# Optimization experiments

Hardware: AMD Instinct MI355X
Metric: run time of the kernel (lower is better)

## Reference

```python
import jax, jax.numpy as jnp
import numpy as np

DT = 0.01
G = 9.81
M = 1.5
E3 = jnp.array([0.0, 0.0, 1.0], dtype=jnp.float32)
K = 8388608


def setup_inputs() -> dict:
    key = jax.random.key(0)
    k1, k2, k3 = jax.random.split(key, 3)
    f = jax.random.normal(k1, (K, 3), dtype=jnp.float32)
    p_0 = jax.random.normal(k2, (3,), dtype=jnp.float32)
    v_0 = jax.random.normal(k3, (3,), dtype=jnp.float32)
    return {"f": f, "p_0": p_0, "v_0": v_0}


def reference(f, p_0, v_0):
    K_ = f.shape[0]
    # Original loop: v[0] uses f[0]; v[i+1] uses f[i]  =>  f index per step: [0, 0, 1, ..., K-2]
    idx = jnp.concatenate([jnp.zeros(1, dtype=jnp.int32), jnp.arange(K_ - 1, dtype=jnp.int32)])
    a = (DT / M) * f[idx] - (DT * G) * E3          # [K,3] per-step velocity increment
    v = v_0[None, :] + jnp.cumsum(a, axis=0)       # [K,3]
    v_prev = jnp.concatenate([v_0[None, :], v[:-1]], axis=0)
    p = p_0[None, :] + (DT / 2) * jnp.cumsum(v + v_prev, axis=0)  # trapezoidal position
    return (p, v)
```

## Files before the change

### kernel.cpp

```cpp
#include <hip/hip_runtime.h>


namespace {
constexpr int  KE    = 8388608;
constexpr int  CHUNK = 2048;
constexpr int  NB    = KE / CHUNK;
constexpr int  BLOCK = 256;
constexpr int  R     = CHUNK / BLOCK;
constexpr int  NF4   = 3 * CHUNK / 4;
constexpr int  PRET  = 1024;
constexpr int  BPT   = NB / PRET;
constexpr float DTc = 0.01f;
constexpr float Cc  = 0.01f / 1.5f;
constexpr float GZ  = -0.01f * 9.81f;
typedef float f32x4 __attribute__((ext_vector_type(4)));
__device__ __forceinline__ int physf4(int q) { return 7 * (q / 6) + q % 6; }
}

__global__ __launch_bounds__(BLOCK) void k_agg(const float* __restrict__ f,
                                               float* __restrict__ W) {
  const int b = blockIdx.x, t = threadIdx.x;
  const int lane = t & 63, wid = t >> 6;
  const float4* src = (const float4*)(f + (size_t)3 * CHUNK * b);
  float A[3] = {0.f, 0.f, 0.f}, Bw[3] = {0.f, 0.f, 0.f};
#pragma unroll
  for (int it = 0; it < 2; ++it) {
    int q3 = it * BLOCK + t;
    float4 d0 = src[3 * q3], d1 = src[3 * q3 + 1], d2 = src[3 * q3 + 2];
    float j0 = (float)(4 * q3), j1 = j0 + 1.f, j2 = j0 + 2.f, j3 = j0 + 3.f;
    A[0] += d0.x; Bw[0] += j0 * d0.x;  A[1] += d0.y; Bw[1] += j0 * d0.y;  A[2] += d0.z; Bw[2] += j0 * d0.z;
    A[0] += d0.w; Bw[0] += j1 * d0.w;  A[1] += d1.x; Bw[1] += j1 * d1.x;  A[2] += d1.y; Bw[2] += j1 * d1.y;
    A[0] += d1.z; Bw[0] += j2 * d1.z;  A[1] += d1.w; Bw[1] += j2 * d1.w;  A[2] += d2.x; Bw[2] += j2 * d2.x;
    A[0] += d2.y; Bw[0] += j3 * d2.y;  A[1] += d2.z; Bw[1] += j3 * d2.z;  A[2] += d2.w; Bw[2] += j3 * d2.w;
  }
#pragma unroll
  for (int d = 32; d >= 1; d >>= 1) {
#pragma unroll
    for (int q = 0; q < 3; ++q) {
      A[q]  += __shfl_down(A[q], d);
      Bw[q] += __shfl_down(Bw[q], d);
    }
  }
  __shared__ float wag[4][6];
  if (lane == 0) {
#pragma unroll
    for (int q = 0; q < 3; ++q) { wag[wid][q] = A[q]; wag[wid][3 + q] = Bw[q]; }
  }
  __syncthreads();
  if (t == 0) {
#pragma unroll
    for (int q = 0; q < 3; ++q) {
      W[q * NB + b]       = wag[0][q] + wag[1][q] + wag[2][q] + wag[3][q];
      W[(3 + q) * NB + b] = wag[0][3 + q] + wag[1][3 + q] + wag[2][3 + q] + wag[3][3 + q];
    }
  }
}

__global__ __launch_bounds__(PRET) void k_pre(const float* __restrict__ W,
                                              float* __restrict__ W2) {
  const int t = threadIdx.x, lane = t & 63, wid = t >> 6;
  double Ac[BPT][3], Wc[BPT][3];
#pragma unroll
  for (int k = 0; k < BPT; ++k) {
    const int c = BPT * t + k;
#pragma unroll
    for (int q = 0; q < 3; ++q) {
      double a  = (double)W[q * NB + c];
      double bw = (double)W[(3 + q) * NB + c];
      Ac[k][q] = a;
      Wc[k][q] = (double)(CHUNK - 1) * a - bw;
    }
  }
  double tA[3] = {0, 0, 0}, tW[3] = {0, 0, 0};
#pragma unroll
  for (int k = 0; k < BPT; ++k) {
#pragma unroll
    for (int q = 0; q < 3; ++q) {
      tW[q] += (double)((BPT - 1 - k) * CHUNK) * Ac[k][q] + Wc[k][q];
      tA[q] += Ac[k][q];
    }
  }
#pragma unroll
  for (int d = 1; d < 64; d <<= 1) {
    double pA[3], pW[3];
#pragma unroll
    for (int q = 0; q < 3; ++q) { pA[q] = __shfl_up(tA[q], d); pW[q] = __shfl_up(tW[q], d); }
    if (lane >= d) {
      const double Ld = (double)(d * BPT * CHUNK);
#pragma unroll
      for (int q = 0; q < 3; ++q) { tW[q] = pW[q] + Ld * pA[q] + tW[q]; tA[q] += pA[q]; }
    }
  }
  double eA[3], eW[3];
#pragma unroll
  for (int q = 0; q < 3; ++q) { eA[q] = __shfl_up(tA[q], 1); eW[q] = __shfl_up(tW[q], 1); }
  if (lane == 0) {
#pragma unroll
    for (int q = 0; q < 3; ++q) { eA[q] = 0.0; eW[q] = 0.0; }
  }
  __shared__ double wagd[16][6];
  if (lane == 63) {
#pragma unroll
    for (int q = 0; q < 3; ++q) { wagd[wid][q] = tA[q]; wagd[wid][3 + q] = tW[q]; }
  }
  __syncthreads();
  double oA[3] = {0, 0, 0}, oW[3] = {0, 0, 0};
  for (int w = 0; w < wid; ++w) {
#pragma unroll
    for (int q = 0; q < 3; ++q) oW[q] = oW[q] + (double)(64 * BPT * CHUNK) * oA[q] + wagd[w][3 + q];
#pragma unroll
    for (int q = 0; q < 3; ++q) oA[q] += wagd[w][q];
  }
  double Ex[3], Hx[3];
#pragma unroll
  for (int q = 0; q < 3; ++q) {
    Ex[q] = oA[q] + eA[q];
    Hx[q] = oW[q] + (double)(lane * BPT * CHUNK) * oA[q] + eW[q];
  }
#pragma unroll
  for (int k = 0; k < BPT; ++k) {
    const int c = BPT * t + k;
#pragma unroll
    for (int q = 0; q < 3; ++q) {
      W2[6 * c + q]     = (float)Ex[q];
      W2[6 * c + 3 + q] = (float)Hx[q];
      Hx[q] += (double)CHUNK * Ex[q] + Wc[k][q];
      Ex[q] += Ac[k][q];
    }
  }
}

__global__ __launch_bounds__(BLOCK, 5) void k_scan(const float* __restrict__ f,
                                                   const float* __restrict__ W2,
                                                   const float* __restrict__ p0v,
                                                   const float* __restrict__ v0v,
                                                   float* __restrict__ out) {
  const int b = blockIdx.x, t = threadIdx.x;
  const int lane = t & 63, wid = t >> 6;
  const long start = (long)b * CHUNK;

  __shared__ f32x4 buf[7 * BLOCK];
  __shared__ float wag[4][6];

  {
    const f32x4* src = (const f32x4*)(f + 3 * start);
#pragma unroll
    for (int it = 0; it < 6; ++it) {
      const int q = t + BLOCK * it;
      buf[physf4(q)] = src[q];
    }
  }
  __syncthreads();

  float z[3 * R];
#pragma unroll
  for (int u = 0; u < 6; ++u) {
    f32x4 d = buf[7 * t + u];
    z[4 * u] = d.x; z[4 * u + 1] = d.y; z[4 * u + 2] = d.z; z[4 * u + 3] = d.w;
  }

  float tS[3] = {0, 0, 0}, tT[3] = {0, 0, 0};
#pragma unroll
  for (int e = 0; e < R; ++e) {
    const float wt = (float)(R - 1 - e);
#pragma unroll
    for (int q = 0; q < 3; ++q) { float v = z[3 * e + q]; tS[q] += v; tT[q] += wt * v; }
  }
#pragma unroll
  for (int d = 1; d < 64; d <<= 1) {
    float pS[3], pT[3];
#pragma unroll
    for (int q = 0; q < 3; ++q) { pS[q] = __shfl_up(tS[q], d); pT[q] = __shfl_up(tT[q], d); }
    if (lane >= d) {
      const float Ld = (float)(R * d);
#pragma unroll
      for (int q = 0; q < 3; ++q) { tT[q] = pT[q] + Ld * pS[q] + tT[q]; tS[q] += pS[q]; }
    }
  }
  float eS[3], eT[3];
#pragma unroll
  for (int q = 0; q < 3; ++q) { eS[q] = __shfl_up(tS[q], 1); eT[q] = __shfl_up(tT[q], 1); }
  if (lane == 0) {
#pragma unroll
    for (int q = 0; q < 3; ++q) { eS[q] = 0.f; eT[q] = 0.f; }
  }
  if (lane == 63) {
#pragma unroll
    for (int q = 0; q < 3; ++q) { wag[wid][q] = tS[q]; wag[wid][3 + q] = tT[q]; }
  }
  __syncthreads();
  float oS[3] = {0, 0, 0}, oT[3] = {0, 0, 0};
  for (int w = 0; w < wid; ++w) {
#pragma unroll
    for (int q = 0; q < 3; ++q) oT[q] = oT[q] + 512.0f * oS[q] + wag[w][3 + q];
#pragma unroll
    for (int q = 0; q < 3; ++q) oS[q] += wag[w][q];
  }
  float E0[3], H0[3];
#pragma unroll
  for (int q = 0; q < 3; ++q) {
    const float Eg = W2[6 * b + q], Hg = W2[6 * b + 3 + q];
    E0[q] = Eg + oS[q] + eS[q];
    H0[q] = Hg + (float)(R * t) * Eg + (oT[q] + (float)(R * lane) * oS[q] + eT[q]);
  }

  const float f0[3] = {f[0], f[1], f[2]};
  const float p0x = p0v[0], p0y = p0v[1], p0z = p0v[2];
  const float v0x = v0v[0], v0y = v0v[1], v0z = v0v[2];
  const float a1 = DTc * Cc, a2 = 0.5f * DTc * Cc, c3 = 0.5f * DTc * GZ;

  float lsum[3] = {0, 0, 0};
  float runH[3] = {H0[0], H0[1], H0[2]};
  float ve[3 * R];
#pragma unroll
  for (int g = 0; g < 2; ++g) {
    float pe[12];
#pragma unroll
    for (int e4 = 0; e4 < 4; ++e4) {
      const int e = 4 * g + e4;
      const float n1 = (float)(int)(start + t * R + e + 1);
      float S_[3], T_[3];
#pragma unroll
      for (int q = 0; q < 3; ++q) {
        const float curE = E0[q] + lsum[q];
        runH[q] += curE;
        S_[q] = f0[q] + curE;
        T_[q] = n1 * f0[q] + runH[q];
        lsum[q] += z[3 * e + q];
      }
      ve[3 * e + 0] = v0x + Cc * S_[0];
      ve[3 * e + 1] = v0y + Cc * S_[1];
      ve[3 * e + 2] = v0z + Cc * S_[2] + GZ * n1;
      pe[3 * e4 + 0] = p0x + DTc * n1 * v0x + a1 * T_[0] - a2 * S_[0];
      pe[3 * e4 + 1] = p0y + DTc * n1 * v0y + a1 * T_[1] - a2 * S_[1];
      pe[3 * e4 + 2] = p0z + DTc * n1 * v0z + a1 * T_[2] - a2 * S_[2] + c3 * n1 * n1;
    }
#pragma unroll
    for (int u = 0; u < 3; ++u) {
      f32x4 pv = {pe[4 * u], pe[4 * u + 1], pe[4 * u + 2], pe[4 * u + 3]};
      buf[7 * t + 3 * g + u] = pv;
    }
  }
  __syncthreads();

  {
    f32x4* dst = (f32x4*)out + (size_t)NF4 * b;
#pragma unroll
    for (int it = 0; it < 6; ++it) {
      const int q = t + BLOCK * it;
      f32x4 d = buf[physf4(q)];
      __builtin_nontemporal_store(d, dst + q);
    }
  }
  __syncthreads();

#pragma unroll
  for (int u = 0; u < 6; ++u) {
    f32x4 vv = {ve[4 * u], ve[4 * u + 1], ve[4 * u + 2], ve[4 * u + 3]};
    buf[7 * t + u] = vv;
  }
  __syncthreads();
  {
    f32x4* dst = (f32x4*)(out + (size_t)3 * KE) + (size_t)NF4 * b;
#pragma unroll
    for (int it = 0; it < 6; ++it) {
      const int q = t + BLOCK * it;
      f32x4 d = buf[physf4(q)];
      __builtin_nontemporal_store(d, dst + q);
    }
  }
}

extern "C" void kernel_launch(void* const* d_in, const int* in_sizes, int n_in,
                              void* d_out, int out_size, void* d_ws, size_t ws_size,
                              hipStream_t stream) {
  const float* f  = (const float*)d_in[0];
  const float* p0 = (const float*)d_in[1];
  const float* v0 = (const float*)d_in[2];
  float* out = (float*)d_out;
  float* W   = (float*)d_ws;
  float* W2  = W + 6 * NB;
  k_agg <<<NB, BLOCK, 0, stream>>>(f, W);
  k_pre <<<1, PRET, 0, stream>>>(W, W2);
  k_scan<<<NB, BLOCK, 0, stream>>>(f, W2, p0, v0, out);
}
```

Before: 75.65 us.

## Halve chunk size, load inputs directly to registers, stage p and v together

Chunk size drops from 2048 to 1024 elements, so each thread handles 4 elements instead of 8 and the grid doubles. The scan kernel now reads f straight from global memory into registers instead of staging it through shared memory, and writes both position and velocity tiles to shared memory in one pass, removing two barriers. k_pre no longer keeps per-chunk values in registers; it re-reads W from global memory in the output loop, cutting register pressure at the cost of extra loads. The direct per-thread loads of 48 contiguous bytes are less coalesced than the old strided pattern, and the larger grid adds launch and block overhead.

```diff
diff --git a/kernel.cpp b/kernel.cpp
--- a/kernel.cpp
+++ b/kernel.cpp
@@ -3,7 +3,7 @@
 
 namespace {
 constexpr int  KE    = 8388608;
-constexpr int  CHUNK = 2048;
+constexpr int  CHUNK = 1024;
 constexpr int  NB    = KE / CHUNK;
 constexpr int  BLOCK = 256;
 constexpr int  R     = CHUNK / BLOCK;
@@ -14,24 +14,20 @@
 constexpr float Cc  = 0.01f / 1.5f;
 constexpr float GZ  = -0.01f * 9.81f;
 typedef float f32x4 __attribute__((ext_vector_type(4)));
-__device__ __forceinline__ int physf4(int q) { return 7 * (q / 6) + q % 6; }
 }
 
 __global__ __launch_bounds__(BLOCK) void k_agg(const float* __restrict__ f,
                                                float* __restrict__ W) {
   const int b = blockIdx.x, t = threadIdx.x;
   const int lane = t & 63, wid = t >> 6;
-  const float4* src = (const float4*)(f + (size_t)3 * CHUNK * b);
-  float A[3] = {0.f, 0.f, 0.f}, Bw[3] = {0.f, 0.f, 0.f};
-#pragma unroll
-  for (int it = 0; it < 2; ++it) {
-    int q3 = it * BLOCK + t;
-    float4 d0 = src[3 * q3], d1 = src[3 * q3 + 1], d2 = src[3 * q3 + 2];
-    float j0 = (float)(4 * q3), j1 = j0 + 1.f, j2 = j0 + 2.f, j3 = j0 + 3.f;
-    A[0] += d0.x; Bw[0] += j0 * d0.x;  A[1] += d0.y; Bw[1] += j0 * d0.y;  A[2] += d0.z; Bw[2] += j0 * d0.z;
-    A[0] += d0.w; Bw[0] += j1 * d0.w;  A[1] += d1.x; Bw[1] += j1 * d1.x;  A[2] += d1.y; Bw[2] += j1 * d1.y;
-    A[0] += d1.z; Bw[0] += j2 * d1.z;  A[1] += d1.w; Bw[1] += j2 * d1.w;  A[2] += d2.x; Bw[2] += j2 * d2.x;
-    A[0] += d2.y; Bw[0] += j3 * d2.y;  A[1] += d2.z; Bw[1] += j3 * d2.z;  A[2] += d2.w; Bw[2] += j3 * d2.w;
+  const f32x4* src = (const f32x4*)(f + (size_t)3 * CHUNK * b);
+  float A[3], Bw[3];
+  {
+    f32x4 d0 = src[3 * t], d1 = src[3 * t + 1], d2 = src[3 * t + 2];
+    const float j0 = (float)(4 * t), j1 = j0 + 1.f, j2 = j0 + 2.f, j3 = j0 + 3.f;
+    A[0] = d0.x + d0.w + d1.z + d2.y;  Bw[0] = j0 * d0.x + j1 * d0.w + j2 * d1.z + j3 * d2.y;
+    A[1] = d0.y + d1.x + d1.w + d2.z;  Bw[1] = j0 * d0.y + j1 * d1.x + j2 * d1.w + j3 * d2.z;
+    A[2] = d0.z + d1.y + d2.x + d2.w;  Bw[2] = j0 * d0.z + j1 * d1.y + j2 * d2.x + j3 * d2.w;
   }
 #pragma unroll
   for (int d = 32; d >= 1; d >>= 1) {
@@ -59,25 +55,17 @@
 __global__ __launch_bounds__(PRET) void k_pre(const float* __restrict__ W,
                                               float* __restrict__ W2) {
   const int t = threadIdx.x, lane = t & 63, wid = t >> 6;
-  double Ac[BPT][3], Wc[BPT][3];
+  double tA[3] = {0, 0, 0}, tW[3] = {0, 0, 0};
 #pragma unroll
   for (int k = 0; k < BPT; ++k) {
     const int c = BPT * t + k;
 #pragma unroll
     for (int q = 0; q < 3; ++q) {
-      double a  = (double)W[q * NB + c];
-      double bw = (double)W[(3 + q) * NB + c];
-      Ac[k][q] = a;
-      Wc[k][q] = (double)(CHUNK - 1) * a - bw;
-    }
-  }
-  double tA[3] = {0, 0, 0}, tW[3] = {0, 0, 0};
-#pragma unroll
-  for (int k = 0; k < BPT; ++k) {
-#pragma unroll
-    for (int q = 0; q < 3; ++q) {
-      tW[q] += (double)((BPT - 1 - k) * CHUNK) * Ac[k][q] + Wc[k][q];
-      tA[q] += Ac[k][q];
+      const double a  = (double)W[q * NB + c];
+      const double bw = (double)W[(3 + q) * NB + c];
+      const double wc = (double)(CHUNK - 1) * a - bw;
+      tW[q] += (double)((BPT - 1 - k) * CHUNK) * a + wc;
+      tA[q] += a;
     }
   }
 #pragma unroll
@@ -124,8 +112,11 @@
     for (int q = 0; q < 3; ++q) {
       W2[6 * c + q]     = (float)Ex[q];
       W2[6 * c + 3 + q] = (float)Hx[q];
-      Hx[q] += (double)CHUNK * Ex[q] + Wc[k][q];
-      Ex[q] += Ac[k][q];
+      const double a  = (double)W[q * NB + c];
+      const double bw = (double)W[(3 + q) * NB + c];
+      const double wc = (double)(CHUNK - 1) * a - bw;
+      Hx[q] += (double)CHUNK * Ex[q] + wc;
+      Ex[q] += a;
     }
   }
 }
@@ -142,21 +133,14 @@
   __shared__ f32x4 buf[7 * BLOCK];
   __shared__ float wag[4][6];
 
-  {
-    const f32x4* src = (const f32x4*)(f + 3 * start);
-#pragma unroll
-    for (int it = 0; it < 6; ++it) {
-      const int q = t + BLOCK * it;
-      buf[physf4(q)] = src[q];
-    }
-  }
-  __syncthreads();
-
   float z[3 * R];
-#pragma unroll
-  for (int u = 0; u < 6; ++u) {
-    f32x4 d = buf[7 * t + u];
-    z[4 * u] = d.x; z[4 * u + 1] = d.y; z[4 * u + 2] = d.z; z[4 * u + 3] = d.w;
+  {
+    const f32x4* src = (const f32x4*)(f + 3 * start) + 3 * t;
+#pragma unroll
+    for (int u = 0; u < 3; ++u) {
+      f32x4 d = src[u];
+      z[4 * u] = d.x; z[4 * u + 1] = d.y; z[4 * u + 2] = d.z; z[4 * u + 3] = d.w;
+    }
   }
 
   float tS[3] = {0, 0, 0}, tT[3] = {0, 0, 0};
@@ -192,7 +176,7 @@
   float oS[3] = {0, 0, 0}, oT[3] = {0, 0, 0};
   for (int w = 0; w < wid; ++w) {
 #pragma unroll
-    for (int q = 0; q < 3; ++q) oT[q] = oT[q] + 512.0f * oS[q] + wag[w][3 + q];
+    for (int q = 0; q < 3; ++q) oT[q] = oT[q] + 256.0f * oS[q] + wag[w][3 + q];
 #pragma unroll
     for (int q = 0; q < 3; ++q) oS[q] += wag[w][q];
   }
@@ -211,61 +195,50 @@
 
   float lsum[3] = {0, 0, 0};
   float runH[3] = {H0[0], H0[1], H0[2]};
-  float ve[3 * R];
-#pragma unroll
-  for (int g = 0; g < 2; ++g) {
-    float pe[12];
-#pragma unroll
-    for (int e4 = 0; e4 < 4; ++e4) {
-      const int e = 4 * g + e4;
-      const float n1 = (float)(int)(start + t * R + e + 1);
-      float S_[3], T_[3];
-#pragma unroll
-      for (int q = 0; q < 3; ++q) {
-        const float curE = E0[q] + lsum[q];
-        runH[q] += curE;
-        S_[q] = f0[q] + curE;
-        T_[q] = n1 * f0[q] + runH[q];
-        lsum[q] += z[3 * e + q];
-      }
-      ve[3 * e + 0] = v0x + Cc * S_[0];
-      ve[3 * e + 1] = v0y + Cc * S_[1];
-      ve[3 * e + 2] = v0z + Cc * S_[2] + GZ * n1;
-      pe[3 * e4 + 0] = p0x + DTc * n1 * v0x + a1 * T_[0] - a2 * S_[0];
-      pe[3 * e4 + 1] = p0y + DTc * n1 * v0y + a1 * T_[1] - a2 * S_[1];
-      pe[3 * e4 + 2] = p0z + DTc * n1 * v0z + a1 * T_[2] - a2 * S_[2] + c3 * n1 * n1;
-    }
-#pragma unroll
-    for (int u = 0; u < 3; ++u) {
-      f32x4 pv = {pe[4 * u], pe[4 * u + 1], pe[4 * u + 2], pe[4 * u + 3]};
-      buf[7 * t + 3 * g + u] = pv;
-    }
+  float pe[12], ve[12];
+#pragma unroll
+  for (int e = 0; e < R; ++e) {
+    const float n1 = (float)(int)(start + t * R + e + 1);
+    float S_[3], T_[3];
+#pragma unroll
+    for (int q = 0; q < 3; ++q) {
+      const float curE = E0[q] + lsum[q];
+      runH[q] += curE;
+      S_[q] = f0[q] + curE;
+      T_[q] = n1 * f0[q] + runH[q];
+      lsum[q] += z[3 * e + q];
+    }
+    ve[3 * e + 0] = v0x + Cc * S_[0];
+    ve[3 * e + 1] = v0y + Cc * S_[1];
+    ve[3 * e + 2] = v0z + Cc * S_[2] + GZ * n1;
+    pe[3 * e + 0] = p0x + DTc * n1 * v0x + a1 * T_[0] - a2 * S_[0];
+    pe[3 * e + 1] = p0y + DTc * n1 * v0y + a1 * T_[1] - a2 * S_[1];
+    pe[3 * e + 2] = p0z + DTc * n1 * v0z + a1 * T_[2] - a2 * S_[2] + c3 * n1 * n1;
+  }
+#pragma unroll
+  for (int u = 0; u < 3; ++u) {
+    f32x4 pv = {pe[4 * u], pe[4 * u + 1], pe[4 * u + 2], pe[4 * u + 3]};
+    f32x4 vv = {ve[4 * u], ve[4 * u + 1], ve[4 * u + 2], ve[4 * u + 3]};
+    buf[7 * t + u]     = pv;
+    buf[7 * t + 3 + u] = vv;
   }
   __syncthreads();
 
   {
     f32x4* dst = (f32x4*)out + (size_t)NF4 * b;
 #pragma unroll
-    for (int it = 0; it < 6; ++it) {
+    for (int it = 0; it < 3; ++it) {
       const int q = t + BLOCK * it;
-      f32x4 d = buf[physf4(q)];
+      f32x4 d = buf[7 * (q / 3) + q % 3];
       __builtin_nontemporal_store(d, dst + q);
     }
   }
-  __syncthreads();
-
-#pragma unroll
-  for (int u = 0; u < 6; ++u) {
-    f32x4 vv = {ve[4 * u], ve[4 * u + 1], ve[4 * u + 2], ve[4 * u + 3]};
-    buf[7 * t + u] = vv;
-  }
-  __syncthreads();
   {
     f32x4* dst = (f32x4*)(out + (size_t)3 * KE) + (size_t)NF4 * b;
 #pragma unroll
-    for (int it = 0; it < 6; ++it) {
+    for (int it = 0; it < 3; ++it) {
       const int q = t + BLOCK * it;
-      f32x4 d = buf[physf4(q)];
+      f32x4 d = buf[7 * (q / 3) + 3 + q % 3];
       __builtin_nontemporal_store(d, dst + q);
     }
   }
```

New measurement: 83.74 us. 10.7% more time.

## Use 512-thread scan blocks with planar LDS staging for p and v

Applied to the files above, without the earlier changes.

The scan kernel now runs 512 threads per block, so each thread handles 4 elements instead of 8. The LDS staging buffer changes from a padded 7-stride layout to three planes per output, which lets p and v be staged together and drops two block barriers plus the second LDS write pass. The larger block raises the wave count and lowers per-thread register pressure. In exchange it uses more LDS per block and adds more cross-wave prefix steps.

```diff
diff --git a/kernel.cpp b/kernel.cpp
--- a/kernel.cpp
+++ b/kernel.cpp
@@ -5,28 +5,29 @@
 constexpr int  KE    = 8388608;
 constexpr int  CHUNK = 2048;
 constexpr int  NB    = KE / CHUNK;
-constexpr int  BLOCK = 256;
-constexpr int  R     = CHUNK / BLOCK;
+constexpr int  ABLK  = 256;
+constexpr int  SBLK  = 512;
+constexpr int  R     = CHUNK / SBLK;
 constexpr int  NF4   = 3 * CHUNK / 4;
+constexpr int  PLANE = NF4 / 3 + 1;
 constexpr int  PRET  = 1024;
 constexpr int  BPT   = NB / PRET;
 constexpr float DTc = 0.01f;
 constexpr float Cc  = 0.01f / 1.5f;
 constexpr float GZ  = -0.01f * 9.81f;
 typedef float f32x4 __attribute__((ext_vector_type(4)));
-__device__ __forceinline__ int physf4(int q) { return 7 * (q / 6) + q % 6; }
-}
-
-__global__ __launch_bounds__(BLOCK) void k_agg(const float* __restrict__ f,
-                                               float* __restrict__ W) {
+}
+
+__global__ __launch_bounds__(ABLK) void k_agg(const float* __restrict__ f,
+                                              float* __restrict__ W) {
   const int b = blockIdx.x, t = threadIdx.x;
   const int lane = t & 63, wid = t >> 6;
-  const float4* src = (const float4*)(f + (size_t)3 * CHUNK * b);
+  const f32x4* src = (const f32x4*)(f + (size_t)3 * CHUNK * b);
   float A[3] = {0.f, 0.f, 0.f}, Bw[3] = {0.f, 0.f, 0.f};
 #pragma unroll
   for (int it = 0; it < 2; ++it) {
-    int q3 = it * BLOCK + t;
-    float4 d0 = src[3 * q3], d1 = src[3 * q3 + 1], d2 = src[3 * q3 + 2];
+    int q3 = it * ABLK + t;
+    f32x4 d0 = src[3 * q3], d1 = src[3 * q3 + 1], d2 = src[3 * q3 + 2];
     float j0 = (float)(4 * q3), j1 = j0 + 1.f, j2 = j0 + 2.f, j3 = j0 + 3.f;
     A[0] += d0.x; Bw[0] += j0 * d0.x;  A[1] += d0.y; Bw[1] += j0 * d0.y;  A[2] += d0.z; Bw[2] += j0 * d0.z;
     A[0] += d0.w; Bw[0] += j1 * d0.w;  A[1] += d1.x; Bw[1] += j1 * d1.x;  A[2] += d1.y; Bw[2] += j1 * d1.y;
@@ -130,32 +131,32 @@
   }
 }
 
-__global__ __launch_bounds__(BLOCK, 5) void k_scan(const float* __restrict__ f,
-                                                   const float* __restrict__ W2,
-                                                   const float* __restrict__ p0v,
-                                                   const float* __restrict__ v0v,
-                                                   float* __restrict__ out) {
+__global__ __launch_bounds__(SBLK, 3) void k_scan(const float* __restrict__ f,
+                                                  const float* __restrict__ W2,
+                                                  const float* __restrict__ p0v,
+                                                  const float* __restrict__ v0v,
+                                                  float* __restrict__ out) {
   const int b = blockIdx.x, t = threadIdx.x;
   const int lane = t & 63, wid = t >> 6;
   const long start = (long)b * CHUNK;
 
-  __shared__ f32x4 buf[7 * BLOCK];
-  __shared__ float wag[4][6];
+  __shared__ f32x4 buf[6 * PLANE];
+  __shared__ float wag[8][6];
 
   {
     const f32x4* src = (const f32x4*)(f + 3 * start);
 #pragma unroll
-    for (int it = 0; it < 6; ++it) {
-      const int q = t + BLOCK * it;
-      buf[physf4(q)] = src[q];
+    for (int it = 0; it < 3; ++it) {
+      const int q = t + SBLK * it;
+      buf[PLANE * (q % 3) + q / 3] = src[q];
     }
   }
   __syncthreads();
 
   float z[3 * R];
 #pragma unroll
-  for (int u = 0; u < 6; ++u) {
-    f32x4 d = buf[7 * t + u];
+  for (int u = 0; u < 3; ++u) {
+    f32x4 d = buf[PLANE * u + t];
     z[4 * u] = d.x; z[4 * u + 1] = d.y; z[4 * u + 2] = d.z; z[4 * u + 3] = d.w;
   }
 
@@ -192,7 +193,7 @@
   float oS[3] = {0, 0, 0}, oT[3] = {0, 0, 0};
   for (int w = 0; w < wid; ++w) {
 #pragma unroll
-    for (int q = 0; q < 3; ++q) oT[q] = oT[q] + 512.0f * oS[q] + wag[w][3 + q];
+    for (int q = 0; q < 3; ++q) oT[q] = oT[q] + 256.0f * oS[q] + wag[w][3 + q];
 #pragma unroll
     for (int q = 0; q < 3; ++q) oS[q] += wag[w][q];
   }
@@ -211,61 +212,50 @@
 
   float lsum[3] = {0, 0, 0};
   float runH[3] = {H0[0], H0[1], H0[2]};
-  float ve[3 * R];
-#pragma unroll
-  for (int g = 0; g < 2; ++g) {
-    float pe[12];
-#pragma unroll
-    for (int e4 = 0; e4 < 4; ++e4) {
-      const int e = 4 * g + e4;
-      const float n1 = (float)(int)(start + t * R + e + 1);
-      float S_[3], T_[3];
-#pragma unroll
-      for (int q = 0; q < 3; ++q) {
-        const float curE = E0[q] + lsum[q];
-        runH[q] += curE;
-        S_[q] = f0[q] + curE;
-        T_[q] = n1 * f0[q] + runH[q];
-        lsum[q] += z[3 * e + q];
-      }
-      ve[3 * e + 0] = v0x + Cc * S_[0];
-      ve[3 * e + 1] = v0y + Cc * S_[1];
-      ve[3 * e + 2] = v0z + Cc * S_[2] + GZ * n1;
-      pe[3 * e4 + 0] = p0x + DTc * n1 * v0x + a1 * T_[0] - a2 * S_[0];
-      pe[3 * e4 + 1] = p0y + DTc * n1 * v0y + a1 * T_[1] - a2 * S_[1];
-      pe[3 * e4 + 2] = p0z + DTc * n1 * v0z + a1 * T_[2] - a2 * S_[2] + c3 * n1 * n1;
-    }
-#pragma unroll
-    for (int u = 0; u < 3; ++u) {
-      f32x4 pv = {pe[4 * u], pe[4 * u + 1], pe[4 * u + 2], pe[4 * u + 3]};
-      buf[7 * t + 3 * g + u] = pv;
-    }
+  float pe[12], ve[12];
+#pragma unroll
+  for (int e = 0; e < R; ++e) {
+    const float n1 = (float)(int)(start + t * R + e + 1);
+    float S_[3], T_[3];
+#pragma unroll
+    for (int q = 0; q < 3; ++q) {
+      const float curE = E0[q] + lsum[q];
+      runH[q] += curE;
+      S_[q] = f0[q] + curE;
+      T_[q] = n1 * f0[q] + runH[q];
+      lsum[q] += z[3 * e + q];
+    }
+    ve[3 * e + 0] = v0x + Cc * S_[0];
+    ve[3 * e + 1] = v0y + Cc * S_[1];
+    ve[3 * e + 2] = v0z + Cc * S_[2] + GZ * n1;
+    pe[3 * e + 0] = p0x + DTc * n1 * v0x + a1 * T_[0] - a2 * S_[0];
+    pe[3 * e + 1] = p0y + DTc * n1 * v0y + a1 * T_[1] - a2 * S_[1];
+    pe[3 * e + 2] = p0z + DTc * n1 * v0z + a1 * T_[2] - a2 * S_[2] + c3 * n1 * n1;
+  }
+#pragma unroll
+  for (int u = 0; u < 3; ++u) {
+    f32x4 pv = {pe[4 * u], pe[4 * u + 1], pe[4 * u + 2], pe[4 * u + 3]};
+    f32x4 vv = {ve[4 * u], ve[4 * u + 1], ve[4 * u + 2], ve[4 * u + 3]};
+    buf[PLANE * u + t]       = pv;
+    buf[PLANE * (3 + u) + t] = vv;
   }
   __syncthreads();
 
   {
     f32x4* dst = (f32x4*)out + (size_t)NF4 * b;
 #pragma unroll
-    for (int it = 0; it < 6; ++it) {
-      const int q = t + BLOCK * it;
-      f32x4 d = buf[physf4(q)];
+    for (int it = 0; it < 3; ++it) {
+      const int q = t + SBLK * it;
+      f32x4 d = buf[PLANE * (q % 3) + q / 3];
       __builtin_nontemporal_store(d, dst + q);
     }
   }
-  __syncthreads();
-
-#pragma unroll
-  for (int u = 0; u < 6; ++u) {
-    f32x4 vv = {ve[4 * u], ve[4 * u + 1], ve[4 * u + 2], ve[4 * u + 3]};
-    buf[7 * t + u] = vv;
-  }
-  __syncthreads();
   {
     f32x4* dst = (f32x4*)(out + (size_t)3 * KE) + (size_t)NF4 * b;
 #pragma unroll
-    for (int it = 0; it < 6; ++it) {
-      const int q = t + BLOCK * it;
-      f32x4 d = buf[physf4(q)];
+    for (int it = 0; it < 3; ++it) {
+      const int q = t + SBLK * it;
+      f32x4 d = buf[PLANE * (3 + q % 3) + q / 3];
       __builtin_nontemporal_store(d, dst + q);
     }
   }
@@ -280,7 +270,7 @@
   float* out = (float*)d_out;
   float* W   = (float*)d_ws;
   float* W2  = W + 6 * NB;
-  k_agg <<<NB, BLOCK, 0, stream>>>(f, W);
+  k_agg <<<NB, ABLK, 0, stream>>>(f, W);
   k_pre <<<1, PRET, 0, stream>>>(W, W2);
-  k_scan<<<NB, BLOCK, 0, stream>>>(f, W2, p0, v0, out);
-}
+  k_scan<<<NB, SBLK, 0, stream>>>(f, W2, p0, v0, out);
+}
```

Result: slower. 78.00 us (+3.1%).

## Fuse chunk aggregation and prefix pass via last-block atomic counter

Applied to the files above, without the earlier changes.

Merges the per-chunk aggregation kernel and the single-block prefix kernel into one launch. Each block publishes its partial sums and increments a global counter, and the last block to arrive does the cross-chunk prefix scan with 256 threads instead of 1024. This removes one kernel launch and its gap, but adds a memset launch, and the serial tail now runs on fewer threads with more work per thread. It also hoists the W2 and scalar loads to the top of the scan kernel so their latency overlaps the shared-memory staging.

```diff
diff --git a/kernel.cpp b/kernel.cpp
--- a/kernel.cpp
+++ b/kernel.cpp
@@ -8,8 +8,7 @@
 constexpr int  BLOCK = 256;
 constexpr int  R     = CHUNK / BLOCK;
 constexpr int  NF4   = 3 * CHUNK / 4;
-constexpr int  PRET  = 1024;
-constexpr int  BPT   = NB / PRET;
+constexpr int  BPT2  = NB / BLOCK;
 constexpr float DTc = 0.01f;
 constexpr float Cc  = 0.01f / 1.5f;
 constexpr float GZ  = -0.01f * 9.81f;
@@ -17,16 +16,19 @@
 __device__ __forceinline__ int physf4(int q) { return 7 * (q / 6) + q % 6; }
 }
 
-__global__ __launch_bounds__(BLOCK) void k_agg(const float* __restrict__ f,
-                                               float* __restrict__ W) {
+__global__ __launch_bounds__(BLOCK) void k_aggpre(const float* __restrict__ f,
+                                                  float* __restrict__ W,
+                                                  float* __restrict__ W2,
+                                                  unsigned int* __restrict__ cnt) {
   const int b = blockIdx.x, t = threadIdx.x;
   const int lane = t & 63, wid = t >> 6;
-  const float4* src = (const float4*)(f + (size_t)3 * CHUNK * b);
+
+  const f32x4* src = (const f32x4*)(f + (size_t)3 * CHUNK * b);
   float A[3] = {0.f, 0.f, 0.f}, Bw[3] = {0.f, 0.f, 0.f};
 #pragma unroll
   for (int it = 0; it < 2; ++it) {
     int q3 = it * BLOCK + t;
-    float4 d0 = src[3 * q3], d1 = src[3 * q3 + 1], d2 = src[3 * q3 + 2];
+    f32x4 d0 = src[3 * q3], d1 = src[3 * q3 + 1], d2 = src[3 * q3 + 2];
     float j0 = (float)(4 * q3), j1 = j0 + 1.f, j2 = j0 + 2.f, j3 = j0 + 3.f;
     A[0] += d0.x; Bw[0] += j0 * d0.x;  A[1] += d0.y; Bw[1] += j0 * d0.y;  A[2] += d0.z; Bw[2] += j0 * d0.z;
     A[0] += d0.w; Bw[0] += j1 * d0.w;  A[1] += d1.x; Bw[1] += j1 * d1.x;  A[2] += d1.y; Bw[2] += j1 * d1.y;
@@ -42,6 +44,7 @@
     }
   }
   __shared__ float wag[4][6];
+  __shared__ int isLast;
   if (lane == 0) {
 #pragma unroll
     for (int q = 0; q < 3; ++q) { wag[wid][q] = A[q]; wag[wid][3 + q] = Bw[q]; }
@@ -50,34 +53,29 @@
   if (t == 0) {
 #pragma unroll
     for (int q = 0; q < 3; ++q) {
-      W[q * NB + b]       = wag[0][q] + wag[1][q] + wag[2][q] + wag[3][q];
-      W[(3 + q) * NB + b] = wag[0][3 + q] + wag[1][3 + q] + wag[2][3 + q] + wag[3][3 + q];
-    }
-  }
-}
-
-__global__ __launch_bounds__(PRET) void k_pre(const float* __restrict__ W,
-                                              float* __restrict__ W2) {
-  const int t = threadIdx.x, lane = t & 63, wid = t >> 6;
-  double Ac[BPT][3], Wc[BPT][3];
-#pragma unroll
-  for (int k = 0; k < BPT; ++k) {
-    const int c = BPT * t + k;
-#pragma unroll
-    for (int q = 0; q < 3; ++q) {
-      double a  = (double)W[q * NB + c];
-      double bw = (double)W[(3 + q) * NB + c];
-      Ac[k][q] = a;
-      Wc[k][q] = (double)(CHUNK - 1) * a - bw;
-    }
-  }
+      float a  = wag[0][q] + wag[1][q] + wag[2][q] + wag[3][q];
+      float bw = wag[0][3 + q] + wag[1][3 + q] + wag[2][3 + q] + wag[3][3 + q];
+      __hip_atomic_store(&W[q * NB + b], a, __ATOMIC_RELAXED, __HIP_MEMORY_SCOPE_AGENT);
+      __hip_atomic_store(&W[(3 + q) * NB + b], bw, __ATOMIC_RELAXED, __HIP_MEMORY_SCOPE_AGENT);
+    }
+    unsigned int old = __hip_atomic_fetch_add(cnt, 1u, __ATOMIC_ACQ_REL, __HIP_MEMORY_SCOPE_AGENT);
+    isLast = (old == (unsigned int)(NB - 1));
+  }
+  __syncthreads();
+  if (!isLast) return;
+
+  __threadfence();
   double tA[3] = {0, 0, 0}, tW[3] = {0, 0, 0};
 #pragma unroll
-  for (int k = 0; k < BPT; ++k) {
-#pragma unroll
-    for (int q = 0; q < 3; ++q) {
-      tW[q] += (double)((BPT - 1 - k) * CHUNK) * Ac[k][q] + Wc[k][q];
-      tA[q] += Ac[k][q];
+  for (int k = 0; k < BPT2; ++k) {
+    const int c = BPT2 * t + k;
+#pragma unroll
+    for (int q = 0; q < 3; ++q) {
+      const double a  = (double)__hip_atomic_load(&W[q * NB + c], __ATOMIC_RELAXED, __HIP_MEMORY_SCOPE_AGENT);
+      const double bw = (double)__hip_atomic_load(&W[(3 + q) * NB + c], __ATOMIC_RELAXED, __HIP_MEMORY_SCOPE_AGENT);
+      const double wc = (double)(CHUNK - 1) * a - bw;
+      tW[q] += (double)((BPT2 - 1 - k) * CHUNK) * a + wc;
+      tA[q] += a;
     }
   }
 #pragma unroll
@@ -86,7 +84,7 @@
 #pragma unroll
     for (int q = 0; q < 3; ++q) { pA[q] = __shfl_up(tA[q], d); pW[q] = __shfl_up(tW[q], d); }
     if (lane >= d) {
-      const double Ld = (double)(d * BPT * CHUNK);
+      const double Ld = (double)(d * BPT2 * CHUNK);
 #pragma unroll
       for (int q = 0; q < 3; ++q) { tW[q] = pW[q] + Ld * pA[q] + tW[q]; tA[q] += pA[q]; }
     }
@@ -98,7 +96,7 @@
 #pragma unroll
     for (int q = 0; q < 3; ++q) { eA[q] = 0.0; eW[q] = 0.0; }
   }
-  __shared__ double wagd[16][6];
+  __shared__ double wagd[4][6];
   if (lane == 63) {
 #pragma unroll
     for (int q = 0; q < 3; ++q) { wagd[wid][q] = tA[q]; wagd[wid][3 + q] = tW[q]; }
@@ -107,7 +105,7 @@
   double oA[3] = {0, 0, 0}, oW[3] = {0, 0, 0};
   for (int w = 0; w < wid; ++w) {
 #pragma unroll
-    for (int q = 0; q < 3; ++q) oW[q] = oW[q] + (double)(64 * BPT * CHUNK) * oA[q] + wagd[w][3 + q];
+    for (int q = 0; q < 3; ++q) oW[q] = oW[q] + (double)(64 * BPT2 * CHUNK) * oA[q] + wagd[w][3 + q];
 #pragma unroll
     for (int q = 0; q < 3; ++q) oA[q] += wagd[w][q];
   }
@@ -115,17 +113,20 @@
 #pragma unroll
   for (int q = 0; q < 3; ++q) {
     Ex[q] = oA[q] + eA[q];
-    Hx[q] = oW[q] + (double)(lane * BPT * CHUNK) * oA[q] + eW[q];
-  }
-#pragma unroll
-  for (int k = 0; k < BPT; ++k) {
-    const int c = BPT * t + k;
+    Hx[q] = oW[q] + (double)(lane * BPT2 * CHUNK) * oA[q] + eW[q];
+  }
+#pragma unroll
+  for (int k = 0; k < BPT2; ++k) {
+    const int c = BPT2 * t + k;
 #pragma unroll
     for (int q = 0; q < 3; ++q) {
       W2[6 * c + q]     = (float)Ex[q];
       W2[6 * c + 3 + q] = (float)Hx[q];
-      Hx[q] += (double)CHUNK * Ex[q] + Wc[k][q];
-      Ex[q] += Ac[k][q];
+      const double a  = (double)__hip_atomic_load(&W[q * NB + c], __ATOMIC_RELAXED, __HIP_MEMORY_SCOPE_AGENT);
+      const double bw = (double)__hip_atomic_load(&W[(3 + q) * NB + c], __ATOMIC_RELAXED, __HIP_MEMORY_SCOPE_AGENT);
+      const double wc = (double)(CHUNK - 1) * a - bw;
+      Hx[q] += (double)CHUNK * Ex[q] + wc;
+      Ex[q] += a;
     }
   }
 }
@@ -139,6 +140,13 @@
   const int lane = t & 63, wid = t >> 6;
   const long start = (long)b * CHUNK;
 
+  float Wg[6];
+#pragma unroll
+  for (int u = 0; u < 6; ++u) Wg[u] = W2[6 * b + u];
+  const float f0[3] = {f[0], f[1], f[2]};
+  const float p0x = p0v[0], p0y = p0v[1], p0z = p0v[2];
+  const float v0x = v0v[0], v0y = v0v[1], v0z = v0v[2];
+
   __shared__ f32x4 buf[7 * BLOCK];
   __shared__ float wag[4][6];
 
@@ -199,16 +207,11 @@
   float E0[3], H0[3];
 #pragma unroll
   for (int q = 0; q < 3; ++q) {
-    const float Eg = W2[6 * b + q], Hg = W2[6 * b + 3 + q];
-    E0[q] = Eg + oS[q] + eS[q];
-    H0[q] = Hg + (float)(R * t) * Eg + (oT[q] + (float)(R * lane) * oS[q] + eT[q]);
-  }
-
-  const float f0[3] = {f[0], f[1], f[2]};
-  const float p0x = p0v[0], p0y = p0v[1], p0z = p0v[2];
-  const float v0x = v0v[0], v0y = v0v[1], v0z = v0v[2];
+    E0[q] = Wg[q] + oS[q] + eS[q];
+    H0[q] = Wg[3 + q] + (float)(R * t) * Wg[q] + (oT[q] + (float)(R * lane) * oS[q] + eT[q]);
+  }
+
   const float a1 = DTc * Cc, a2 = 0.5f * DTc * Cc, c3 = 0.5f * DTc * GZ;
-
   float lsum[3] = {0, 0, 0};
   float runH[3] = {H0[0], H0[1], H0[2]};
   float ve[3 * R];
@@ -278,9 +281,10 @@
   const float* p0 = (const float*)d_in[1];
   const float* v0 = (const float*)d_in[2];
   float* out = (float*)d_out;
-  float* W   = (float*)d_ws;
+  unsigned int* cnt = (unsigned int*)d_ws;
+  float* W   = (float*)d_ws + 16;
   float* W2  = W + 6 * NB;
-  k_agg <<<NB, BLOCK, 0, stream>>>(f, W);
-  k_pre <<<1, PRET, 0, stream>>>(W, W2);
-  k_scan<<<NB, BLOCK, 0, stream>>>(f, W2, p0, v0, out);
-}
+  hipMemsetAsync(cnt, 0, sizeof(unsigned int), stream);
+  k_aggpre<<<NB, BLOCK, 0, stream>>>(f, W, W2, cnt);
+  k_scan  <<<NB, BLOCK, 0, stream>>>(f, W2, p0, v0, out);
+}
```

New measurement: 223.8 us. 2.96x slower.
